# Kernel optimization log

Hardware: AMD Instinct MI355X
Metric: run time of the kernel (lower is better)

## Reference

```python
import jax, jax.numpy as jnp
import numpy as np

N_NODES = 1_000_000
E = 262_144
N_FEAT_COLS = 9        # columns 1..9 of x
CARD = 50_000          # cardinality of each feature embedding table
EMB = 128
EDGE_DIM = 27
# node type (col 0) that activates each feature column h (h = col index - 1):
# files (type 0) use cols 1..4, processes (type 1) use col 5, sockets (type 2) use cols 6..9
TYPE_PER_COL = (0, 0, 0, 0, 1, 2, 2, 2, 2)


def setup_inputs() -> dict:
    key = jax.random.key(0)
    ks = jax.random.split(key, 10)
    type_col = jax.random.randint(ks[0], (N_NODES, 1), 0, 3, dtype=jnp.int32)
    feat_cols = jax.random.randint(ks[1], (N_NODES, N_FEAT_COLS), 0, CARD, dtype=jnp.int32)
    x = jnp.concatenate([type_col, feat_cols], axis=1)  # [N_NODES, 10]
    src = jax.random.randint(ks[2], (E,), 0, N_NODES, dtype=jnp.int32)
    dst = jax.random.randint(ks[3], (E,), 0, N_NODES, dtype=jnp.int32)
    neg_dst = jax.random.randint(ks[4], (E,), 0, N_NODES, dtype=jnp.int32)
    msg = jax.random.normal(ks[5], (E, EDGE_DIM), dtype=jnp.float32)
    emb_type = jax.random.normal(ks[6], (3, EMB), dtype=jnp.float32)            # embeddings[0]
    emb_feats = jax.random.normal(ks[7], (N_FEAT_COLS, CARD, EMB), dtype=jnp.float32)  # embeddings[1..9]
    edge_w = jax.random.normal(ks[8], (EMB, EDGE_DIM), dtype=jnp.float32) / np.sqrt(EDGE_DIM)
    edge_b = jnp.zeros((EMB,), dtype=jnp.float32)
    out_w = jax.random.normal(ks[9], (1, EMB), dtype=jnp.float32) / np.sqrt(EMB)
    out_b = jnp.zeros((1,), dtype=jnp.float32)
    return dict(x=x, src=src, dst=dst, neg_dst=neg_dst, msg=msg,
                emb_type=emb_type, emb_feats=emb_feats,
                edge_w=edge_w, edge_b=edge_b, out_w=out_w, out_b=out_b)


def _encode_features(rows, emb_type, emb_feats):
    """rows: [E,10] int. Equivalent to torch encode_features: per node type,
    sum the type-specific embedding lookups; col-0 (type) embedding is shared."""
    t = rows[:, 0]                     # [E] node type
    out = emb_type[t]                  # embeddings[0] applies to every type
    for h in range(N_FEAT_COLS):       # small fixed loop over 9 tables
        mask = (t == TYPE_PER_COL[h]).astype(out.dtype)[:, None]   # [E,1]
        out = out + emb_feats[h][rows[:, h + 1]] * mask            # masked gather-sum
    return out                         # [E, EMB]


def reference(x, src, dst, neg_dst, msg, emb_type, emb_feats, edge_w, edge_b, out_w, out_b):
    h_src = _encode_features(x[src], emb_type, emb_feats)       # [E, EMB]
    h_pos_dst = _encode_features(x[dst], emb_type, emb_feats)
    h_neg_dst = _encode_features(x[neg_dst], emb_type, emb_feats)
    target_msg = msg @ edge_w.T + edge_b                        # Linear(edge_dim -> EMB)
    h_pos_edge = jax.nn.relu(h_src + h_pos_dst)
    h_neg_edge = jax.nn.relu(h_src + h_neg_dst)
    pos = (h_pos_edge + target_msg) @ out_w.T + out_b           # [E, 1]
    neg = (h_neg_edge + target_msg) @ out_w.T + out_b           # [E, 1]
    return (pos, neg)
```

## Files before the change

### kernel.cpp

```cpp
#include <hip/hip_runtime.h>

#define NUM_EDGES 262144
#define CARD 50000
#define EMB 128
#define EDGE_DIM 27

__global__ void prep_kernel(const float* __restrict__ edge_w,
                            const float* __restrict__ edge_b,
                            const float* __restrict__ out_w,
                            const float* __restrict__ out_b,
                            float* __restrict__ ws) {
    int j = threadIdx.x;
    if (j < EDGE_DIM) {
        float s = 0.f;
        for (int k = 0; k < EMB; ++k) s += out_w[k] * edge_w[k * EDGE_DIM + j];
        ws[j] = s;
    } else if (j == EDGE_DIM) {
        float s = out_b[0];
        for (int k = 0; k < EMB; ++k) s += edge_b[k] * out_w[k];
        ws[EDGE_DIM] = s;
    }
}

__global__ __launch_bounds__(256, 4) void edge_pred_kernel(
    const int* __restrict__ x, const int* __restrict__ src,
    const int* __restrict__ dst, const int* __restrict__ neg_dst,
    const float* __restrict__ msg, const float* __restrict__ emb_type,
    const float* __restrict__ emb_feats, const float* __restrict__ out_w,
    const float* __restrict__ ws, float* __restrict__ out) {
    const int lane = threadIdx.x & 63;
    const int wave = threadIdx.x >> 6;
    const int e0 = __builtin_amdgcn_readfirstlane(blockIdx.x * 8 + wave * 2);

    const int half = lane >> 5;
    const int hl = lane & 31;
    const int loff = lane * 2;

    int nodes[6];
    nodes[0] = src[e0];     nodes[1] = dst[e0];     nodes[2] = neg_dst[e0];
    nodes[3] = src[e0 + 1]; nodes[4] = dst[e0 + 1]; nodes[5] = neg_dst[e0 + 1];

    float mterm = 0.f;
    if (hl < EDGE_DIM) {
        mterm = __builtin_nontemporal_load(msg + (size_t)(e0 + half) * EDGE_DIM + hl) * ws[hl];
    }

    float2 v[6][5];
    float wpad[6];
#pragma unroll
    for (int n = 0; n < 6; ++n) {
        const int* xr = x + (size_t)nodes[n] * 10;
        const int t = xr[0];
        const int c1 = xr[1], c2 = xr[2], c3 = xr[3], c4 = xr[4], c5 = xr[5],
                  c6 = xr[6], c7 = xr[7], c8 = xr[8], c9 = xr[9];
        const int i0 = (t == 0) ? c1 : (t == 1) ? c5 : c6;
        const int i1 = (t == 0) ? c2 : (t == 1) ? c5 : c7;
        const int i2 = (t == 0) ? c3 : (t == 1) ? c5 : c8;
        const int i3 = (t == 0) ? c4 : (t == 1) ? c5 : c9;
        const int h0 = (t == 0) ? 0 : (t == 1) ? 4 : 5;
        const int h1 = (t == 0) ? 1 : (t == 1) ? 4 : 6;
        const int h2 = (t == 0) ? 2 : (t == 1) ? 4 : 7;
        const int h3 = (t == 0) ? 3 : (t == 1) ? 4 : 8;
        wpad[n] = (t == 1) ? 0.f : 1.f;

        v[n][0] = *(const float2*)(emb_type + (size_t)t * EMB + loff);
        v[n][1] = *(const float2*)(emb_feats + ((size_t)h0 * CARD + (size_t)i0) * EMB + loff);
        v[n][2] = *(const float2*)(emb_feats + ((size_t)h1 * CARD + (size_t)i1) * EMB + loff);
        v[n][3] = *(const float2*)(emb_feats + ((size_t)h2 * CARD + (size_t)i2) * EMB + loff);
        v[n][4] = *(const float2*)(emb_feats + ((size_t)h3 * CARD + (size_t)i3) * EMB + loff);
    }
    const float2 wv = *(const float2*)(out_w + loff);

    __builtin_amdgcn_sched_barrier(0);

    float hx[6], hy[6];
#pragma unroll
    for (int n = 0; n < 6; ++n) {
        const float ax = v[n][0].x + v[n][1].x;
        const float ay = v[n][0].y + v[n][1].y;
        const float bx = v[n][2].x + v[n][3].x + v[n][4].x;
        const float by = v[n][2].y + v[n][3].y + v[n][4].y;
        hx[n] = ax + wpad[n] * bx;
        hy[n] = ay + wpad[n] * by;
    }

    float p0 = fmaxf(hx[0] + hx[1], 0.f) * wv.x + fmaxf(hy[0] + hy[1], 0.f) * wv.y;
    float q0 = fmaxf(hx[0] + hx[2], 0.f) * wv.x + fmaxf(hy[0] + hy[2], 0.f) * wv.y;
    float p1 = fmaxf(hx[3] + hx[4], 0.f) * wv.x + fmaxf(hy[3] + hy[4], 0.f) * wv.y;
    float q1 = fmaxf(hx[3] + hx[5], 0.f) * wv.x + fmaxf(hy[3] + hy[5], 0.f) * wv.y;

    if (half == 0) { p0 += mterm; q0 += mterm; }
    else           { p1 += mterm; q1 += mterm; }

    p0 += __shfl_xor(p0, 32, 64);
    q0 += __shfl_xor(q0, 32, 64);
    p1 += __shfl_xor(p1, 32, 64);
    q1 += __shfl_xor(q1, 32, 64);
    float pz = half ? p1 : p0;
    float qz = half ? q1 : q0;
#pragma unroll
    for (int off = 16; off > 0; off >>= 1) {
        pz += __shfl_xor(pz, off, 64);
        qz += __shfl_xor(qz, off, 64);
    }

    if (hl == 0) {
        const float b2 = ws[EDGE_DIM];
        const int e = e0 + half;
        out[e] = pz + b2;
        out[NUM_EDGES + e] = qz + b2;
    }
}

extern "C" void kernel_launch(void* const* d_in, const int* in_sizes, int n_in,
                              void* d_out, int out_size, void* d_ws, size_t ws_size,
                              hipStream_t stream) {
    const int* x = (const int*)d_in[0];
    const int* src = (const int*)d_in[1];
    const int* dst = (const int*)d_in[2];
    const int* neg_dst = (const int*)d_in[3];
    const float* msg = (const float*)d_in[4];
    const float* emb_type = (const float*)d_in[5];
    const float* emb_feats = (const float*)d_in[6];
    const float* edge_w = (const float*)d_in[7];
    const float* edge_b = (const float*)d_in[8];
    const float* out_w = (const float*)d_in[9];
    const float* out_b = (const float*)d_in[10];
    float* out = (float*)d_out;
    float* ws = (float*)d_ws;

    prep_kernel<<<1, 64, 0, stream>>>(edge_w, edge_b, out_w, out_b, ws);

    const int blocks = NUM_EDGES / 8;
    edge_pred_kernel<<<blocks, 256, 0, stream>>>(x, src, dst, neg_dst, msg,
                                                 emb_type, emb_feats, out_w, ws,
                                                 out);
}
```

Measured before the change: 508.5 us.

## Convert embedding tables to fp16 and pre-pack node rows before gathering

Each call now adds a pass that converts all nine feature embedding tables to fp16 in workspace. A second pre-pass packs each node's type, pad flag and four resolved table indices into a single 16-byte record. The edge kernel then gathers half-width embedding rows and one packed record per node instead of ten ints, which halves the gather bytes and removes the per-node index selection. In exchange, every call pays a full read of the fp32 tables and of x, embedding values lose precision, and the new path only runs when the workspace is large enough.

```diff
diff --git a/kernel.cpp b/kernel.cpp
--- a/kernel.cpp
+++ b/kernel.cpp
@@ -1,9 +1,19 @@
 #include <hip/hip_runtime.h>
-
+#include <hip/hip_fp16.h>
+
+#define N_NODES 1000000
 #define NUM_EDGES 262144
 #define CARD 50000
 #define EMB 128
 #define EDGE_DIM 27
+
+typedef float vfloat4 __attribute__((ext_vector_type(4)));
+typedef unsigned int vuint4 __attribute__((ext_vector_type(4)));
+
+#define XPACK_OFF 4096
+#define EMB16_OFF (XPACK_OFF + (size_t)N_NODES * 16)
+#define EMB_ELEMS (9ull * CARD * EMB)
+#define WS_NEEDED (EMB16_OFF + EMB_ELEMS * 2)
 
 __global__ void prep_kernel(const float* __restrict__ edge_w,
                             const float* __restrict__ edge_b,
@@ -19,6 +29,147 @@
         float s = out_b[0];
         for (int k = 0; k < EMB; ++k) s += edge_b[k] * out_w[k];
         ws[EDGE_DIM] = s;
+    }
+}
+
+__global__ __launch_bounds__(256) void pack_x_kernel(const int* __restrict__ x,
+                                                     uint4* __restrict__ xp) {
+    int i = blockIdx.x * 256 + threadIdx.x;
+    if (i >= N_NODES) return;
+    const int* r = x + (size_t)i * 10;
+    const int t  = __builtin_nontemporal_load(r + 0);
+    const int c1 = __builtin_nontemporal_load(r + 1);
+    const int c2 = __builtin_nontemporal_load(r + 2);
+    const int c3 = __builtin_nontemporal_load(r + 3);
+    const int c4 = __builtin_nontemporal_load(r + 4);
+    const int c5 = __builtin_nontemporal_load(r + 5);
+    const int c6 = __builtin_nontemporal_load(r + 6);
+    const int c7 = __builtin_nontemporal_load(r + 7);
+    const int c8 = __builtin_nontemporal_load(r + 8);
+    const int c9 = __builtin_nontemporal_load(r + 9);
+    unsigned i0, i1, i2, i3, pad = 0;
+    if (t == 0) {
+        i0 = (unsigned)c1;
+        i1 = 1u * CARD + (unsigned)c2;
+        i2 = 2u * CARD + (unsigned)c3;
+        i3 = 3u * CARD + (unsigned)c4;
+    } else if (t == 1) {
+        i0 = i1 = i2 = i3 = 4u * CARD + (unsigned)c5;
+        pad = 1u;
+    } else {
+        i0 = 5u * CARD + (unsigned)c6;
+        i1 = 6u * CARD + (unsigned)c7;
+        i2 = 7u * CARD + (unsigned)c8;
+        i3 = 8u * CARD + (unsigned)c9;
+    }
+    uint4 o;
+    o.x = i0 | ((unsigned)t << 20) | (pad << 22);
+    o.y = i1;
+    o.z = i2;
+    o.w = i3;
+    xp[i] = o;
+}
+
+__global__ __launch_bounds__(256) void cvt_emb_kernel(const float* __restrict__ src,
+                                                      __half* __restrict__ dst) {
+    size_t i = ((size_t)blockIdx.x * 256 + threadIdx.x) * 8;
+    vfloat4 a = __builtin_nontemporal_load((const vfloat4*)(src + i));
+    vfloat4 b = __builtin_nontemporal_load((const vfloat4*)(src + i + 4));
+    __half2 h0 = __floats2half2_rn(a.x, a.y);
+    __half2 h1 = __floats2half2_rn(a.z, a.w);
+    __half2 h2 = __floats2half2_rn(b.x, b.y);
+    __half2 h3 = __floats2half2_rn(b.z, b.w);
+    vuint4 o;
+    o.x = *(unsigned*)&h0;
+    o.y = *(unsigned*)&h1;
+    o.z = *(unsigned*)&h2;
+    o.w = *(unsigned*)&h3;
+    *(vuint4*)(dst + i) = o;
+}
+
+__global__ __launch_bounds__(256, 4) void edge_pred_fp16(
+    const uint4* __restrict__ xp, const int* __restrict__ src,
+    const int* __restrict__ dst, const int* __restrict__ neg_dst,
+    const float* __restrict__ msg, const float* __restrict__ emb_type,
+    const __half* __restrict__ e16, const float* __restrict__ out_w,
+    const float* __restrict__ ws, float* __restrict__ out) {
+    const int lane = threadIdx.x & 63;
+    const int wave = threadIdx.x >> 6;
+    const int e0 = __builtin_amdgcn_readfirstlane(blockIdx.x * 8 + wave * 2);
+
+    const int half = lane >> 5;
+    const int hl = lane & 31;
+    const int loff = lane * 2;
+
+    int nodes[6];
+    nodes[0] = src[e0];     nodes[1] = dst[e0];     nodes[2] = neg_dst[e0];
+    nodes[3] = src[e0 + 1]; nodes[4] = dst[e0 + 1]; nodes[5] = neg_dst[e0 + 1];
+
+    float mterm = 0.f;
+    if (hl < EDGE_DIM) {
+        mterm = __builtin_nontemporal_load(msg + (size_t)(e0 + half) * EDGE_DIM + hl) * ws[hl];
+    }
+
+    float2 v0[6];
+    unsigned u[6][4];
+    float wpad[6];
+#pragma unroll
+    for (int n = 0; n < 6; ++n) {
+        const uint4 px = xp[nodes[n]];
+        const unsigned t = (px.x >> 20) & 3u;
+        wpad[n] = (px.x & (1u << 22)) ? 0.f : 1.f;
+        const size_t i0 = (size_t)(px.x & 0xFFFFFu);
+
+        v0[n] = *(const float2*)(emb_type + (size_t)t * EMB + loff);
+        u[n][0] = *(const unsigned*)((const char*)e16 + (i0 * EMB + loff) * 2);
+        u[n][1] = *(const unsigned*)((const char*)e16 + ((size_t)px.y * EMB + loff) * 2);
+        u[n][2] = *(const unsigned*)((const char*)e16 + ((size_t)px.z * EMB + loff) * 2);
+        u[n][3] = *(const unsigned*)((const char*)e16 + ((size_t)px.w * EMB + loff) * 2);
+    }
+    const float2 wv = *(const float2*)(out_w + loff);
+
+    __builtin_amdgcn_sched_barrier(0);
+
+    float hx[6], hy[6];
+#pragma unroll
+    for (int n = 0; n < 6; ++n) {
+        const float2 f1 = __half22float2(*(const __half2*)&u[n][0]);
+        const float2 f2 = __half22float2(*(const __half2*)&u[n][1]);
+        const float2 f3 = __half22float2(*(const __half2*)&u[n][2]);
+        const float2 f4 = __half22float2(*(const __half2*)&u[n][3]);
+        const float ax = v0[n].x + f1.x;
+        const float ay = v0[n].y + f1.y;
+        const float bx = f2.x + f3.x + f4.x;
+        const float by = f2.y + f3.y + f4.y;
+        hx[n] = ax + wpad[n] * bx;
+        hy[n] = ay + wpad[n] * by;
+    }
+
+    float p0 = fmaxf(hx[0] + hx[1], 0.f) * wv.x + fmaxf(hy[0] + hy[1], 0.f) * wv.y;
+    float q0 = fmaxf(hx[0] + hx[2], 0.f) * wv.x + fmaxf(hy[0] + hy[2], 0.f) * wv.y;
+    float p1 = fmaxf(hx[3] + hx[4], 0.f) * wv.x + fmaxf(hy[3] + hy[4], 0.f) * wv.y;
+    float q1 = fmaxf(hx[3] + hx[5], 0.f) * wv.x + fmaxf(hy[3] + hy[5], 0.f) * wv.y;
+
+    if (half == 0) { p0 += mterm; q0 += mterm; }
+    else           { p1 += mterm; q1 += mterm; }
+
+    p0 += __shfl_xor(p0, 32, 64);
+    q0 += __shfl_xor(q0, 32, 64);
+    p1 += __shfl_xor(p1, 32, 64);
+    q1 += __shfl_xor(q1, 32, 64);
+    float pz = half ? p1 : p0;
+    float qz = half ? q1 : q0;
+#pragma unroll
+    for (int off = 16; off > 0; off >>= 1) {
+        pz += __shfl_xor(pz, off, 64);
+        qz += __shfl_xor(qz, off, 64);
+    }
+
+    if (hl == 0) {
+        const float b2 = ws[EDGE_DIM];
+        const int e = e0 + half;
+        out[e] = pz + b2;
+        out[NUM_EDGES + e] = qz + b2;
     }
 }
 
@@ -132,7 +283,17 @@
     prep_kernel<<<1, 64, 0, stream>>>(edge_w, edge_b, out_w, out_b, ws);
 
     const int blocks = NUM_EDGES / 8;
-    edge_pred_kernel<<<blocks, 256, 0, stream>>>(x, src, dst, neg_dst, msg,
-                                                 emb_type, emb_feats, out_w, ws,
-                                                 out);
-}
+
+    if (ws_size >= WS_NEEDED) {
+        uint4* xp = (uint4*)((char*)d_ws + XPACK_OFF);
+        __half* e16 = (__half*)((char*)d_ws + EMB16_OFF);
+        pack_x_kernel<<<(N_NODES + 255) / 256, 256, 0, stream>>>(x, xp);
+        cvt_emb_kernel<<<28125, 256, 0, stream>>>(emb_feats, e16);
+        edge_pred_fp16<<<blocks, 256, 0, stream>>>(xp, src, dst, neg_dst, msg,
+                                                   emb_type, e16, out_w, ws, out);
+    } else {
+        edge_pred_kernel<<<blocks, 256, 0, stream>>>(x, src, dst, neg_dst, msg,
+                                                     emb_type, emb_feats, out_w,
+                                                     ws, out);
+    }
+}
```

Result: faster. 473.9 us (-6.8%).
